# Performance work log

Hardware: AMD Instinct MI355X
Metric: run time of the kernel (lower is better)

## Reference

```python
import jax, jax.numpy as jnp
import numpy as np


def setup_inputs() -> dict:
    key = jax.random.key(0)
    n, d = 256, 64
    ks = jax.random.split(key, 8)
    x = jax.random.normal(ks[0], (n, d), jnp.float32)
    v = jax.random.normal(ks[1], (n, d), jnp.float32)
    # torch nn.Linear convention: weight shape (out_features, in_features)
    W1 = jax.random.normal(ks[2], (d, d), jnp.float32) * (1.0 / np.sqrt(d))
    b1 = jax.random.normal(ks[3], (d,), jnp.float32) * 0.1
    # W2 scaled small + b2 ~ scaled identity so g = M + M^T is well-conditioned (invertible)
    W2 = jax.random.normal(ks[4], (d * d, d), jnp.float32) * 0.02
    b2 = (3.0 * jnp.eye(d, dtype=jnp.float32)).reshape(d * d) \
         + jax.random.normal(ks[5], (d * d,), jnp.float32) * 0.01
    W3 = jax.random.normal(ks[6], (d, 2 * d), jnp.float32) * (1.0 / np.sqrt(2 * d))
    return {"t": 0, "x": x, "v": v, "W1": W1, "b1": b1, "W2": W2, "b2": b2, "W3": W3}


def reference(t, x, v, W1, b1, W2, b2, W3):
    # Connection_gnew.forward. t is unused (ODE-time placeholder), matching the original.
    n, d = x.shape
    # g network: linear1 -> tanh -> linear2 -> symmetrize
    h = jnp.tanh(x @ W1.T + b1)                      # (n, d)
    M = (h @ W2.T + b2).reshape(n, d, d)             # (n, d, d)
    g = M + jnp.transpose(M, (0, 2, 1))              # symmetric metric (n, d, d)
    g_inv = jnp.linalg.inv(g)
    # Analytic batch jacobian of g_flat wrt x (replaces autograd.functional.jacobian):
    # d M_flat[a]/d x[l] = sum_m W2[a,m] * (1 - h[m]^2) * W1[m,l]; then symmetrize (i<->j).
    s = 1.0 - h * h                                   # tanh' (n, d)
    J = jnp.einsum('am,nm,ml->nal', W2, s, W1).reshape(n, d, d, d)
    J = J + jnp.transpose(J, (0, 2, 1, 3))            # J[n,i,j,l] = d g_{ij} / d x_l
    # einsum('nkl,nijl,njil,nlij->nkij', g_inv, J, J, -J):
    # elementwise triple product over matching indices, then contract l with g_inv.
    T = J * jnp.transpose(J, (0, 2, 1, 3)) * (-jnp.transpose(J, (0, 2, 3, 1)))  # T[n,i,j,l]
    connection = 0.5 * jnp.einsum('nkl,nijl->nkij', g_inv, T)
    # dv[n,k] = -sum_{ij} v_i v_j connection[n,k,i,j]
    dv = -jnp.einsum('ni,nj,nkij->nk', v, v, connection)
    out = jnp.concatenate([v, dv], axis=-1) @ W3.T    # linear3, no bias
    return out
```

## Files before the change

kernel.cpp:

```cpp
#include <hip/hip_runtime.h>
#include <math.h>
#include <stdint.h>


typedef short short8 __attribute__((ext_vector_type(8)));
typedef float f32x4 __attribute__((ext_vector_type(4)));

__device__ __forceinline__ unsigned short f2bf(float f) {
  unsigned int u = __builtin_bit_cast(unsigned int, f);
  u += 0x7fffu + ((u >> 16) & 1u);
  return (unsigned short)(u >> 16);
}

__device__ __forceinline__ short8 as_short8(uint4 u) {
  union { uint4 a; short8 b; } cv; cv.a = u; return cv.b;
}

__global__ __launch_bounds__(256) void prep_w2s_kernel(const float* __restrict__ W2,
                                                       unsigned short* __restrict__ W2sB) {
  int idx = blockIdx.x * 256 + threadIdx.x;
  int i = idx >> 12, j = (idx >> 6) & 63, m = idx & 63;
  W2sB[idx] = f2bf(W2[(((i << 6) + j) << 6) + m] + W2[(((j << 6) + i) << 6) + m]);
}

__global__ __launch_bounds__(256) void conn_kernel(
    const float* __restrict__ x, const float* __restrict__ v,
    const float* __restrict__ W1, const float* __restrict__ b1,
    const float* __restrict__ b2, const float* __restrict__ W3,
    const unsigned short* __restrict__ W2sB, float* __restrict__ out) {
  __shared__ __align__(16) unsigned short sKT[80 * 80];
  __shared__ __align__(16) float jit[2][64 * 68];
  __shared__ float sg[64 * 65];
  __shared__ float spq[64 * 16];
  __shared__ float sh[64], sv[64], sx[64], sq[64], sz[64];

  const int n = blockIdx.x, t = threadIdx.x;
  const int wv = t >> 6, lane = t & 63, ln15 = lane & 15, quad = lane >> 4;
  const int j0 = 16 * wv + 4 * quad;
  const int arow = 16 * wv + ln15;

  if (t < 64) { sx[t] = x[(n << 6) + t]; sv[t] = v[(n << 6) + t]; }
  for (int e = t; e < 6400; e += 256) sKT[e] = 0;
  __syncthreads();

  if (t < 64) {
    float acc = b1[t];
    #pragma unroll 8
    for (int l = 0; l < 64; ++l) acc += sx[l] * W1[(t << 6) + l];
    sh[t] = tanhf(acc);
  }
  __syncthreads();

  for (int e = t; e < 4096; e += 256) {
    int m = e & 63, l = e >> 6;
    float hm = sh[m];
    sKT[l * 80 + m] = f2bf((1.f - hm * hm) * W1[(m << 6) + l]);
  }
  if (t < 64) sKT[64 * 80 + t] = f2bf(sh[t]);
  __syncthreads();

  short8 bf[5][2];
  #pragma unroll
  for (int lc = 0; lc < 5; ++lc)
    #pragma unroll
    for (int ks = 0; ks < 2; ++ks)
      bf[lc][ks] = *(const short8*)&sKT[(lc * 16 + ln15) * 80 + ks * 32 + quad * 8];

  float svj[4];
  #pragma unroll
  for (int r = 0; r < 4; ++r) svj[r] = sv[j0 + r];

  f32x4 c[5];
  float qacc[4] = {0.f, 0.f, 0.f, 0.f};

  const unsigned short* abase = W2sB + (arow << 6) + quad * 8;
  uint4 a0 = *(const uint4*)(abase);
  uint4 a1 = *(const uint4*)(abase + 32);

  for (int i = 0; i < 64; ++i) {
    const unsigned short* anext = abase + (((size_t)((i + 1) & 63)) << 12);
    uint4 an0 = *(const uint4*)(anext);
    uint4 an1 = *(const uint4*)(anext + 32);

    if (i > 0) {
      const float* jp = jit[(i - 1) & 1];
      float vi = sv[i - 1];
      #pragma unroll
      for (int lc = 0; lc < 4; ++lc) {
        float acc = 0.f;
        #pragma unroll
        for (int r = 0; r < 4; ++r) {
          float cj = c[lc][r];
          float jt = jp[(j0 + r) * 68 + lc * 16 + ln15];
          acc += svj[r] * cj * cj * jt;
        }
        qacc[lc] += vi * acc;
      }
    }

    short8 A0 = as_short8(a0), A1 = as_short8(a1);
    #pragma unroll
    for (int lc = 0; lc < 5; ++lc) {
      f32x4 z4 = {0.f, 0.f, 0.f, 0.f};
      f32x4 cc = __builtin_amdgcn_mfma_f32_16x16x32_bf16(A0, bf[lc][0], z4, 0, 0, 0);
      c[lc]    = __builtin_amdgcn_mfma_f32_16x16x32_bf16(A1, bf[lc][1], cc, 0, 0, 0);
    }

    float* jw = jit[i & 1];
    #pragma unroll
    for (int lc = 0; lc < 4; ++lc)
      *(f32x4*)&jw[(lc * 16 + ln15) * 68 + j0] = c[lc];
    if (ln15 == 0) {
      #pragma unroll
      for (int r = 0; r < 4; ++r) sg[i * 65 + j0 + r] = c[4][r];
    }
    __syncthreads();
    a0 = an0; a1 = an1;
  }

  {
    const float* jp = jit[1];
    float vi = sv[63];
    #pragma unroll
    for (int lc = 0; lc < 4; ++lc) {
      float acc = 0.f;
      #pragma unroll
      for (int r = 0; r < 4; ++r) {
        float cj = c[lc][r];
        float jt = jp[(j0 + r) * 68 + lc * 16 + ln15];
        acc += svj[r] * cj * cj * jt;
      }
      qacc[lc] += vi * acc;
    }
  }
  #pragma unroll
  for (int lc = 0; lc < 4; ++lc)
    spq[(lc * 16 + ln15) * 16 + (wv * 4 + quad)] = qacc[lc];

  for (int e = t; e < 4096; e += 256) {
    int r = e >> 6, cc2 = e & 63;
    sg[r * 65 + cc2] += b2[(r << 6) + cc2] + b2[(cc2 << 6) + r];
  }
  __syncthreads();

  if (t < 64) {
    float s = 0.f;
    #pragma unroll
    for (int e2 = 0; e2 < 16; ++e2) s += spq[t * 16 + e2];
    sq[t] = s;
    sz[t] = s / sg[t * 65 + t];
  }
  __syncthreads();

  {
    const int r = 16 * wv + ln15;
    const float* grow = &sg[r * 65];
    const float dinv = 1.f / grow[r];
    const float qr = sq[r];
    for (int it = 0; it < 20; ++it) {
      float p = 0.f;
      #pragma unroll
      for (int cc2 = 0; cc2 < 16; ++cc2) {
        int cidx = quad * 16 + cc2;
        p += grow[cidx] * sz[cidx];
      }
      p += __shfl_xor(p, 16, 64);
      p += __shfl_xor(p, 32, 64);
      float zr = 0.f;
      if (quad == 0) zr = sz[r] + (qr - p) * dinv;
      __syncthreads();
      if (quad == 0) sz[r] = zr;
      __syncthreads();
    }
  }

  if (t < 64) {
    float accv = 0.f, accd = 0.f;
    #pragma unroll 8
    for (int c2 = 0; c2 < 64; ++c2) {
      accv += sv[c2] * W3[(t << 7) + c2];
      accd += sz[c2] * W3[(t << 7) + 64 + c2];
    }
    out[(n << 6) + t] = accv + 0.5f * accd;
  }
}

extern "C" void kernel_launch(void* const* d_in, const int* in_sizes, int n_in,
                              void* d_out, int out_size, void* d_ws, size_t ws_size,
                              hipStream_t stream) {
  (void)in_sizes; (void)n_in; (void)out_size; (void)ws_size;
  const float* x  = (const float*)d_in[1];
  const float* v  = (const float*)d_in[2];
  const float* W1 = (const float*)d_in[3];
  const float* b1 = (const float*)d_in[4];
  const float* W2 = (const float*)d_in[5];
  const float* b2 = (const float*)d_in[6];
  const float* W3 = (const float*)d_in[7];
  unsigned short* W2sB = (unsigned short*)d_ws;

  hipLaunchKernelGGL(prep_w2s_kernel, dim3(1024), dim3(256), 0, stream, W2, W2sB);
  hipLaunchKernelGGL(conn_kernel, dim3(256), dim3(256), 0, stream,
                     x, v, W1, b1, b2, W3, W2sB, (float*)d_out);
}
```

Measured before the change: 110.8 us.

## Compute transposed Jacobian tiles in registers, drop per-row LDS exchange and barriers

```diff
diff --git a/kernel.cpp b/kernel.cpp
--- a/kernel.cpp
+++ b/kernel.cpp
@@ -23,21 +23,18 @@
   W2sB[idx] = f2bf(W2[(((i << 6) + j) << 6) + m] + W2[(((j << 6) + i) << 6) + m]);
 }
 
-__global__ __launch_bounds__(256) void conn_kernel(
+__global__ __launch_bounds__(256, 1) void conn_kernel(
     const float* __restrict__ x, const float* __restrict__ v,
     const float* __restrict__ W1, const float* __restrict__ b1,
     const float* __restrict__ b2, const float* __restrict__ W3,
     const unsigned short* __restrict__ W2sB, float* __restrict__ out) {
   __shared__ __align__(16) unsigned short sKT[80 * 80];
-  __shared__ __align__(16) float jit[2][64 * 68];
-  __shared__ float sg[64 * 65];
-  __shared__ float spq[64 * 16];
-  __shared__ float sh[64], sv[64], sx[64], sq[64], sz[64];
+  __shared__ __align__(16) float sg[64 * 68];
+  __shared__ float spq[4][64];
+  __shared__ __align__(16) float sh[64], sv[64], sx[64], sq[64], sz[64];
 
   const int n = blockIdx.x, t = threadIdx.x;
   const int wv = t >> 6, lane = t & 63, ln15 = lane & 15, quad = lane >> 4;
-  const int j0 = 16 * wv + 4 * quad;
-  const int arow = 16 * wv + ln15;
 
   if (t < 64) { sx[t] = x[(n << 6) + t]; sv[t] = v[(n << 6) + t]; }
   for (int e = t; e < 6400; e += 256) sKT[e] = 0;
@@ -61,107 +58,104 @@
 
   short8 bf[5][2];
   #pragma unroll
-  for (int lc = 0; lc < 5; ++lc)
+  for (int tc = 0; tc < 5; ++tc)
     #pragma unroll
     for (int ks = 0; ks < 2; ++ks)
-      bf[lc][ks] = *(const short8*)&sKT[(lc * 16 + ln15) * 80 + ks * 32 + quad * 8];
+      bf[tc][ks] = *(const short8*)&sKT[(tc * 16 + ln15) * 80 + ks * 32 + quad * 8];
 
-  float svj[4];
+  f32x4 svj[4];
   #pragma unroll
-  for (int r = 0; r < 4; ++r) svj[r] = sv[j0 + r];
+  for (int tr = 0; tr < 4; ++tr) svj[tr] = *(const f32x4*)&sv[tr * 16 + quad * 4];
 
-  f32x4 c[5];
   float qacc[4] = {0.f, 0.f, 0.f, 0.f};
 
-  const unsigned short* abase = W2sB + (arow << 6) + quad * 8;
-  uint4 a0 = *(const uint4*)(abase);
-  uint4 a1 = *(const uint4*)(abase + 32);
+  const int foff = (ln15 << 6) + quad * 8;
+  const unsigned short* sbase = W2sB + ((size_t)(16 * wv) << 12);
 
-  for (int i = 0; i < 64; ++i) {
-    const unsigned short* anext = abase + (((size_t)((i + 1) & 63)) << 12);
-    uint4 an0 = *(const uint4*)(anext);
-    uint4 an1 = *(const uint4*)(anext + 32);
+  uint4 af[4][2], afn[4][2];
+  #pragma unroll
+  for (int tc = 0; tc < 4; ++tc) {
+    af[tc][0] = *(const uint4*)(sbase + (tc << 10) + foff);
+    af[tc][1] = *(const uint4*)(sbase + (tc << 10) + foff + 32);
+  }
 
-    if (i > 0) {
-      const float* jp = jit[(i - 1) & 1];
-      float vi = sv[i - 1];
+  for (int ii = 0; ii < 16; ++ii) {
+    const unsigned short* spn = W2sB + ((size_t)(16 * wv + ((ii + 1) & 15)) << 12);
+    #pragma unroll
+    for (int tc = 0; tc < 4; ++tc) {
+      afn[tc][0] = *(const uint4*)(spn + (tc << 10) + foff);
+      afn[tc][1] = *(const uint4*)(spn + (tc << 10) + foff + 32);
+    }
+    const int i = 16 * wv + ii;
+    const float vi = sv[i];
+
+    #pragma unroll
+    for (int tr = 0; tr < 4; ++tr) {
+      short8 a0 = as_short8(af[tr][0]), a1 = as_short8(af[tr][1]);
+      f32x4 c1[4], c2[4], ce;
       #pragma unroll
-      for (int lc = 0; lc < 4; ++lc) {
-        float acc = 0.f;
+      for (int tc = 0; tc < 4; ++tc) {
+        f32x4 z4 = {0.f, 0.f, 0.f, 0.f};
+        f32x4 u = __builtin_amdgcn_mfma_f32_16x16x32_bf16(a0, bf[tc][0], z4, 0, 0, 0);
+        c1[tc]  = __builtin_amdgcn_mfma_f32_16x16x32_bf16(a1, bf[tc][1], u, 0, 0, 0);
+        f32x4 w = __builtin_amdgcn_mfma_f32_16x16x32_bf16(bf[tr][0], as_short8(af[tc][0]), z4, 0, 0, 0);
+        c2[tc]  = __builtin_amdgcn_mfma_f32_16x16x32_bf16(bf[tr][1], as_short8(af[tc][1]), w, 0, 0, 0);
+      }
+      {
+        f32x4 z4 = {0.f, 0.f, 0.f, 0.f};
+        f32x4 u = __builtin_amdgcn_mfma_f32_16x16x32_bf16(a0, bf[4][0], z4, 0, 0, 0);
+        ce      = __builtin_amdgcn_mfma_f32_16x16x32_bf16(a1, bf[4][1], u, 0, 0, 0);
+      }
+      if (ln15 == 0)
+        *(f32x4*)&sg[i * 68 + tr * 16 + quad * 4] = ce;
+
+      #pragma unroll
+      for (int tc = 0; tc < 4; ++tc) {
+        float s = 0.f;
         #pragma unroll
         for (int r = 0; r < 4; ++r) {
-          float cj = c[lc][r];
-          float jt = jp[(j0 + r) * 68 + lc * 16 + ln15];
-          acc += svj[r] * cj * cj * jt;
+          float a = c1[tc][r];
+          s = fmaf(a * a * c2[tc][r], svj[tr][r], s);
         }
-        qacc[lc] += vi * acc;
+        qacc[tc] = fmaf(s, vi, qacc[tc]);
       }
     }
-
-    short8 A0 = as_short8(a0), A1 = as_short8(a1);
     #pragma unroll
-    for (int lc = 0; lc < 5; ++lc) {
-      f32x4 z4 = {0.f, 0.f, 0.f, 0.f};
-      f32x4 cc = __builtin_amdgcn_mfma_f32_16x16x32_bf16(A0, bf[lc][0], z4, 0, 0, 0);
-      c[lc]    = __builtin_amdgcn_mfma_f32_16x16x32_bf16(A1, bf[lc][1], cc, 0, 0, 0);
-    }
-
-    float* jw = jit[i & 1];
-    #pragma unroll
-    for (int lc = 0; lc < 4; ++lc)
-      *(f32x4*)&jw[(lc * 16 + ln15) * 68 + j0] = c[lc];
-    if (ln15 == 0) {
-      #pragma unroll
-      for (int r = 0; r < 4; ++r) sg[i * 65 + j0 + r] = c[4][r];
-    }
-    __syncthreads();
-    a0 = an0; a1 = an1;
+    for (int tc = 0; tc < 4; ++tc) { af[tc][0] = afn[tc][0]; af[tc][1] = afn[tc][1]; }
   }
 
-  {
-    const float* jp = jit[1];
-    float vi = sv[63];
-    #pragma unroll
-    for (int lc = 0; lc < 4; ++lc) {
-      float acc = 0.f;
-      #pragma unroll
-      for (int r = 0; r < 4; ++r) {
-        float cj = c[lc][r];
-        float jt = jp[(j0 + r) * 68 + lc * 16 + ln15];
-        acc += svj[r] * cj * cj * jt;
-      }
-      qacc[lc] += vi * acc;
-    }
+  #pragma unroll
+  for (int tc = 0; tc < 4; ++tc) {
+    float s = qacc[tc];
+    s += __shfl_xor(s, 16, 64);
+    s += __shfl_xor(s, 32, 64);
+    if (quad == 0) spq[wv][tc * 16 + ln15] = s;
   }
-  #pragma unroll
-  for (int lc = 0; lc < 4; ++lc)
-    spq[(lc * 16 + ln15) * 16 + (wv * 4 + quad)] = qacc[lc];
+  __syncthreads();
 
   for (int e = t; e < 4096; e += 256) {
-    int r = e >> 6, cc2 = e & 63;
-    sg[r * 65 + cc2] += b2[(r << 6) + cc2] + b2[(cc2 << 6) + r];
+    int r = e >> 6, c = e & 63;
+    sg[r * 68 + c] += b2[(r << 6) + c] + b2[(c << 6) + r];
   }
   __syncthreads();
 
   if (t < 64) {
-    float s = 0.f;
-    #pragma unroll
-    for (int e2 = 0; e2 < 16; ++e2) s += spq[t * 16 + e2];
+    float s = spq[0][t] + spq[1][t] + spq[2][t] + spq[3][t];
     sq[t] = s;
-    sz[t] = s / sg[t * 65 + t];
+    sz[t] = s / sg[t * 68 + t];
   }
   __syncthreads();
 
   {
     const int r = 16 * wv + ln15;
-    const float* grow = &sg[r * 65];
+    const float* grow = &sg[r * 68];
     const float dinv = 1.f / grow[r];
     const float qr = sq[r];
     for (int it = 0; it < 20; ++it) {
       float p = 0.f;
       #pragma unroll
-      for (int cc2 = 0; cc2 < 16; ++cc2) {
-        int cidx = quad * 16 + cc2;
+      for (int cc = 0; cc < 16; ++cc) {
+        int cidx = quad * 16 + cc;
         p += grow[cidx] * sz[cidx];
       }
       p += __shfl_xor(p, 16, 64);
@@ -177,9 +171,9 @@
   if (t < 64) {
     float accv = 0.f, accd = 0.f;
     #pragma unroll 8
-    for (int c2 = 0; c2 < 64; ++c2) {
-      accv += sv[c2] * W3[(t << 7) + c2];
-      accd += sz[c2] * W3[(t << 7) + 64 + c2];
+    for (int c = 0; c < 64; ++c) {
+      accv += sv[c] * W3[(t << 7) + c];
+      accd += sz[c] * W3[(t << 7) + 64 + c];
     }
     out[(n << 6) + t] = accv + 0.5f * accd;
   }
```

New measurement: 103.0 us. -7.0%, faster.
